# Kernel optimization log

Hardware: AMD Instinct MI355X
Metric: run time of the kernel (lower is better)

Reference implementation:

```python
import jax, jax.numpy as jnp
import numpy as np

B, C, H, W = 64, 256, 32, 32
HID = C // 16          # SE hidden = channels // ratio
EMB = 16               # channel/snr embed dim
COND = 2 * EMB         # cond vector dim = 32
RHID = 64              # rate controller hidden
SNR_DB = 10.0
CH_IDX = 2             # 'Combined_channel'
POWER = 2.0
BASE_CR, MIN_CR, MAX_CR, ALPHA = 0.5, 0.3, 1.0, 0.7


def setup_inputs() -> dict:
    key = jax.random.key(0)
    ks = jax.random.split(key, 16)
    g = lambda k, sh: (jax.random.normal(k, sh, dtype=jnp.float32) * 0.05)
    return {
        "x": jax.random.normal(ks[0], (B, C, H, W), dtype=jnp.float32),
        "channel_embed": g(ks[1], (3, EMB)),
        "snr_w1": g(ks[2], (EMB, 1)), "snr_b1": jnp.zeros((EMB,), jnp.float32),
        "snr_w2": g(ks[3], (EMB, EMB)), "snr_b2": jnp.zeros((EMB,), jnp.float32),
        "base_w1": g(ks[4], (HID, C)),
        "base_w2": g(ks[5], (C, HID)),
        "sem_proj": g(ks[6], (HID, C)),
        "cond_proj": g(ks[7], (HID, COND)),
        "out_proj": g(ks[8], (C, HID)),
        "r_w1": g(ks[9], (RHID, C + COND)), "r_b1": jnp.zeros((RHID,), jnp.float32),
        "r_w2": g(ks[10], (RHID, RHID)), "r_b2": jnp.zeros((RHID,), jnp.float32),
        "r_w3": g(ks[11], (1, RHID)), "r_b3": jnp.zeros((1,), jnp.float32),
    }


def _topk_mask(weights, k):
    # weights [B,C], k [B] int; keep top-k per row (vectorized rank trick).
    order = jnp.argsort(-weights, axis=1)
    ranks = jnp.argsort(order, axis=1)
    return (ranks < k[:, None]).astype(weights.dtype)


def reference(x, channel_embed, snr_w1, snr_b1, snr_w2, snr_b2,
              base_w1, base_w2, sem_proj, cond_proj, out_proj,
              r_w1, r_b1, r_w2, r_b2, r_w3, r_b3):
    b, c, h, w = x.shape
    sem = x.mean(axis=(2, 3))                                   # [B,C] GAP
    # channel condition encoder
    ch_vec = jnp.broadcast_to(channel_embed[CH_IDX], (b, EMB))
    s_in = jnp.full((b, 1), SNR_DB / 28.0, dtype=x.dtype)
    sv = jax.nn.relu(s_in @ snr_w1.T + snr_b1)
    sv = jax.nn.relu(sv @ snr_w2.T + snr_b2)
    cond = jnp.concatenate([ch_vec, sv], axis=1)                # [B,32]
    # base SE weights * channel-conditioned gate
    base = jax.nn.sigmoid(jax.nn.relu(sem @ base_w1.T) @ base_w2.T)
    gate = jax.nn.sigmoid(jax.nn.relu(sem @ sem_proj.T + cond @ cond_proj.T) @ out_proj.T)
    weights = base * gate                                       # [B,C]
    # rate controller -> per-sample cr
    r = jax.nn.relu(jnp.concatenate([sem, cond], axis=1) @ r_w1.T + r_b1)
    r = jax.nn.relu(r @ r_w2.T + r_b2)
    raw = jax.nn.sigmoid(r @ r_w3.T + r_b3)[:, 0]
    dyn = MIN_CR + (MAX_CR - MIN_CR) * raw
    cr = jnp.clip((1.0 - ALPHA) * BASE_CR + ALPHA * dyn, MIN_CR, MAX_CR)
    k = jnp.clip(jnp.round(cr * c).astype(jnp.int32), 1, c)
    mask = _topk_mask(weights, k)
    z = x * (weights * mask)[:, :, None, None]                  # masked latent
    # --- combined channel: flat Rayleigh fading + per-(b,c,h) AWGN ---
    F = c * h * w
    zf = z.reshape(b, F)
    xr, xi = zf[:, 0::2], zf[:, 1::2]                           # [B,F/2]
    nk = jax.random.split(jax.random.key(42), 5)
    hr = jax.random.normal(nk[0], xr.shape, x.dtype)            # torch h_i (real)
    hi = jax.random.normal(nk[1], xr.shape, x.dtype)            # torch h_r (imag)
    std = jnp.sqrt(jnp.asarray(POWER / (10.0 ** (SNR_DB / 10.0)), x.dtype))
    nr = std * jax.random.normal(nk[2], xr.shape, x.dtype)
    ni = std * jax.random.normal(nk[3], xr.shape, x.dtype)
    yr = hr * xr - hi * xi + nr
    yi = hr * xi + hi * xr + ni
    den = hr * hr + hi * hi
    outr = (yr * hr + yi * hi) / den
    outi = (yi * hr - yr * hi) / den
    faded = jnp.stack([outr, outi], axis=-1).reshape(b, c, h, w)
    # per-(b,c,h) random SNR map AWGN
    kk = jax.random.split(nk[4], 2)
    snr_map = jax.random.randint(kk[0], (b, c, h, 1), 0, 29).astype(x.dtype)
    std2 = jnp.sqrt(POWER / (10.0 ** (snr_map / 10.0)))
    return faded + std2 * jax.random.normal(kk[1], (b, c, h, w), x.dtype)
```

## Files before the change

### kernel.cpp

```cpp
#include <hip/hip_runtime.h>

#define NB 64
#define NC 256
#define NF 262144
#define NPAIR 131072
#define NROWS 524288

struct U2 { unsigned a, b; };

__host__ __device__ constexpr unsigned rotl32(unsigned x, int d) {
  return (x << d) | (x >> (32 - d));
}

__host__ __device__ constexpr U2 tf2x32(unsigned k0, unsigned k1,
                                        unsigned x0, unsigned x1) {
  const unsigned ks0 = k0, ks1 = k1, ks2 = k0 ^ k1 ^ 0x1BD11BDAu;
  x0 += ks0; x1 += ks1;
  x0 += x1; x1 = rotl32(x1, 13); x1 ^= x0;
  x0 += x1; x1 = rotl32(x1, 15); x1 ^= x0;
  x0 += x1; x1 = rotl32(x1, 26); x1 ^= x0;
  x0 += x1; x1 = rotl32(x1, 6);  x1 ^= x0;
  x0 += ks1; x1 += ks2 + 1u;
  x0 += x1; x1 = rotl32(x1, 17); x1 ^= x0;
  x0 += x1; x1 = rotl32(x1, 29); x1 ^= x0;
  x0 += x1; x1 = rotl32(x1, 16); x1 ^= x0;
  x0 += x1; x1 = rotl32(x1, 24); x1 ^= x0;
  x0 += ks2; x1 += ks0 + 2u;
  x0 += x1; x1 = rotl32(x1, 13); x1 ^= x0;
  x0 += x1; x1 = rotl32(x1, 15); x1 ^= x0;
  x0 += x1; x1 = rotl32(x1, 26); x1 ^= x0;
  x0 += x1; x1 = rotl32(x1, 6);  x1 ^= x0;
  x0 += ks0; x1 += ks1 + 3u;
  x0 += x1; x1 = rotl32(x1, 17); x1 ^= x0;
  x0 += x1; x1 = rotl32(x1, 29); x1 ^= x0;
  x0 += x1; x1 = rotl32(x1, 16); x1 ^= x0;
  x0 += x1; x1 = rotl32(x1, 24); x1 ^= x0;
  x0 += ks1; x1 += ks2 + 4u;
  x0 += x1; x1 = rotl32(x1, 13); x1 ^= x0;
  x0 += x1; x1 = rotl32(x1, 15); x1 ^= x0;
  x0 += x1; x1 = rotl32(x1, 26); x1 ^= x0;
  x0 += x1; x1 = rotl32(x1, 6);  x1 ^= x0;
  x0 += ks2; x1 += ks0 + 5u;
  return U2{x0, x1};
}

constexpr U2 NK0 = tf2x32(0u, 42u, 0u, 0u);
constexpr U2 NK1 = tf2x32(0u, 42u, 0u, 1u);
constexpr U2 NK2 = tf2x32(0u, 42u, 0u, 2u);
constexpr U2 NK3 = tf2x32(0u, 42u, 0u, 3u);
constexpr U2 NK4 = tf2x32(0u, 42u, 0u, 4u);
constexpr U2 KK0 = tf2x32(NK4.a, NK4.b, 0u, 0u);
constexpr U2 KK1 = tf2x32(NK4.a, NK4.b, 0u, 1u);

__device__ __forceinline__ unsigned rb32(unsigned k0, unsigned k1, unsigned m) {
  const unsigned ks2 = k0 ^ k1 ^ 0x1BD11BDAu;
  unsigned x0 = k0, x1 = m + k1;
#define QR(r) x0 += x1; x1 = __builtin_rotateleft32(x1, r); x1 ^= x0;
  QR(13) QR(15) QR(26) QR(6)
  x0 += k1;  x1 += ks2 + 1u;
  QR(17) QR(29) QR(16) QR(24)
  x0 += ks2; x1 += k0 + 2u;
  QR(13) QR(15) QR(26) QR(6)
  x0 += k0;  x1 += k1 + 3u;
  QR(17) QR(29) QR(16) QR(24)
  x0 += k1;  x1 += ks2 + 4u;
  QR(13) QR(15) QR(26) QR(6)
  x0 += ks2; x1 += k0 + 5u;
#undef QR
  return x0 ^ x1;
}

__device__ __forceinline__ float normal_fast(unsigned bits) {
  const float lo = __uint_as_float(0xBF7FFFFFu);
  float u = __uint_as_float((bits >> 9) | 0x3F800000u) - 1.0f;
  float v = fmaf(u, 2.0f, lo);
  float t = fmaf(-v, v, 1.0f);
  float w = __builtin_amdgcn_logf(t) * -0.69314718f;
  float p;
  if (w < 5.0f) {
    float z = w - 2.5f;
    p = 2.81022636e-08f;
    p = fmaf(p, z, 3.43273939e-07f);
    p = fmaf(p, z, -3.5233877e-06f);
    p = fmaf(p, z, -4.39150654e-06f);
    p = fmaf(p, z, 0.00021858087f);
    p = fmaf(p, z, -0.00125372503f);
    p = fmaf(p, z, -0.00417768164f);
    p = fmaf(p, z, 0.246640727f);
    p = fmaf(p, z, 1.50140941f);
  } else {
    float z = __builtin_amdgcn_sqrtf(w) - 3.0f;
    p = -0.000200214257f;
    p = fmaf(p, z, 0.000100950558f);
    p = fmaf(p, z, 0.00134934322f);
    p = fmaf(p, z, -0.00367342844f);
    p = fmaf(p, z, 0.00573950773f);
    p = fmaf(p, z, -0.0076224613f);
    p = fmaf(p, z, 0.00943887047f);
    p = fmaf(p, z, 1.00167406f);
    p = fmaf(p, z, 2.83297682f);
  }
  return 1.41421356f * (p * v);
}

__global__ __launch_bounds__(256) void snr_kernel(float* __restrict__ std2) {
  const unsigned j = blockIdx.x * 256u + threadIdx.x;
  unsigned hb = rb32(KK0.a, KK0.b, j);
  unsigned lb = rb32(KK0.a, KK0.b, NROWS + j);
  unsigned snr = ((hb % 29u) * 16u + (lb % 29u)) % 29u;
  std2[j] = __builtin_amdgcn_sqrtf(
      2.0f * __builtin_amdgcn_exp2f((float)snr * -0.33219281f));
}

__global__ __launch_bounds__(256) void sem_kernel(const float* __restrict__ x,
                                                  float* __restrict__ sem) {
  int row = (blockIdx.x * 256 + threadIdx.x) >> 6;
  int lane = threadIdx.x & 63;
  const float* rp = x + (size_t)row * 1024;
  float acc = 0.0f;
#pragma unroll
  for (int i = 0; i < 4; ++i) {
    float4 v = *(const float4*)(rp + i * 256 + lane * 4);
    acc += v.x + v.y + v.z + v.w;
  }
#pragma unroll
  for (int off = 32; off > 0; off >>= 1) acc += __shfl_down(acc, off, 64);
  if (lane == 0) sem[row] = acc * (1.0f / 1024.0f);
}

__global__ __launch_bounds__(256) void head_kernel(
    const float* __restrict__ sem_g, const float* __restrict__ channel_embed,
    const float* __restrict__ snr_w1, const float* __restrict__ snr_b1,
    const float* __restrict__ snr_w2, const float* __restrict__ snr_b2,
    const float* __restrict__ base_w1, const float* __restrict__ base_w2,
    const float* __restrict__ sem_proj, const float* __restrict__ cond_proj,
    const float* __restrict__ out_proj, const float* __restrict__ r_w1,
    const float* __restrict__ r_b1, const float* __restrict__ r_w2,
    const float* __restrict__ r_b2, const float* __restrict__ r_w3,
    const float* __restrict__ r_b3, float* __restrict__ s_out) {
  __shared__ float sem_s[256];
  __shared__ float sv1_s[16];
  __shared__ float cond_s[32];
  __shared__ float hid_s[16], g1_s[16];
  __shared__ float r1_s[64], r2_s[64];
  __shared__ float w_s[256];
  __shared__ int k_s;
  const int b = blockIdx.x, t = threadIdx.x;

  sem_s[t] = sem_g[b * 256 + t];
  if (t < 16) {
    const float s_in = (float)(10.0 / 28.0);
    sv1_s[t] = fmaxf(0.0f, s_in * snr_w1[t] + snr_b1[t]);
  }
  __syncthreads();
  if (t < 16) {
    float a = snr_b2[t];
    for (int f = 0; f < 16; ++f) a += sv1_s[f] * snr_w2[t * 16 + f];
    cond_s[16 + t] = fmaxf(0.0f, a);
    cond_s[t] = channel_embed[2 * 16 + t];
  }
  __syncthreads();
  if (t < 16) {
    float a1 = 0.0f, a2 = 0.0f;
    for (int c = 0; c < 256; ++c) {
      float sc = sem_s[c];
      a1 += sc * base_w1[t * 256 + c];
      a2 += sc * sem_proj[t * 256 + c];
    }
    for (int j = 0; j < 32; ++j) a2 += cond_s[j] * cond_proj[t * 32 + j];
    hid_s[t] = fmaxf(0.0f, a1);
    g1_s[t] = fmaxf(0.0f, a2);
  } else if (t < 80) {
    int i = t - 16;
    float a = r_b1[i];
    for (int c = 0; c < 256; ++c) a += sem_s[c] * r_w1[i * 288 + c];
    for (int j = 0; j < 32; ++j) a += cond_s[j] * r_w1[i * 288 + 256 + j];
    r1_s[i] = fmaxf(0.0f, a);
  }
  __syncthreads();
  if (t < 64) {
    float a = r_b2[t];
    for (int j = 0; j < 64; ++j) a += r1_s[j] * r_w2[t * 64 + j];
    r2_s[t] = fmaxf(0.0f, a);
  }
  {
    float a1 = 0.0f, a2 = 0.0f;
    for (int i = 0; i < 16; ++i) {
      a1 += hid_s[i] * base_w2[t * 16 + i];
      a2 += g1_s[i] * out_proj[t * 16 + i];
    }
    float base = 1.0f / (1.0f + expf(-a1));
    float gate = 1.0f / (1.0f + expf(-a2));
    w_s[t] = base * gate;
  }
  __syncthreads();
  if (t == 0) {
    float a = r_b3[0];
    for (int j = 0; j < 64; ++j) a += r2_s[j] * r_w3[j];
    float raw = 1.0f / (1.0f + expf(-a));
    float dyn = 0.3f + 0.7f * raw;
    float cr = 0.15f + 0.7f * dyn;
    cr = fminf(fmaxf(cr, 0.3f), 1.0f);
    int k = (int)rintf(cr * 256.0f);
    k_s = min(max(k, 1), 256);
  }
  __syncthreads();
  {
    float wc = w_s[t];
    int cnt = 0;
    for (int j = 0; j < 256; ++j) {
      float wj = w_s[j];
      cnt += (wj > wc) || (wj == wc && j < t);
    }
    s_out[b * 256 + t] = (cnt < k_s) ? wc : 0.0f;
  }
}

__global__ __launch_bounds__(256) void sim_kernel(const float* __restrict__ x,
                                                  const float* __restrict__ s,
                                                  const float* __restrict__ std2v,
                                                  float* __restrict__ out) {
  const unsigned tid = blockIdx.x * 256u + threadIdx.x;
  const unsigned q0 = tid * 8u;

  const float4 xa = *(const float4*)(x + q0);
  const float4 xb = *(const float4*)(x + q0 + 4);
  const float sc = s[q0 >> 10];
  const float std2 = std2v[q0 >> 5];

  const unsigned m0 = tid * 4u;
  float hr[4], hi[4], nr[4], ni[4], n2[8];
  const float STD = 0.44721359f;
#pragma unroll
  for (int i = 0; i < 4; ++i) hr[i] = normal_fast(rb32(NK0.a, NK0.b, m0 + i));
#pragma unroll
  for (int i = 0; i < 4; ++i) hi[i] = normal_fast(rb32(NK1.a, NK1.b, m0 + i));
#pragma unroll
  for (int i = 0; i < 4; ++i)
    nr[i] = STD * normal_fast(rb32(NK2.a, NK2.b, m0 + i));
#pragma unroll
  for (int i = 0; i < 4; ++i)
    ni[i] = STD * normal_fast(rb32(NK3.a, NK3.b, m0 + i));
#pragma unroll
  for (int i = 0; i < 8; ++i) n2[i] = normal_fast(rb32(KK1.a, KK1.b, q0 + i));

  float xs[8] = {xa.x * sc, xa.y * sc, xa.z * sc, xa.w * sc,
                 xb.x * sc, xb.y * sc, xb.z * sc, xb.w * sc};
  float o[8];
#pragma unroll
  for (int i = 0; i < 4; ++i) {
    const float den = fmaf(hr[i], hr[i], hi[i] * hi[i]);
    const float rc = __builtin_amdgcn_rcpf(den);
    o[2 * i] = fmaf(fmaf(hr[i], nr[i], hi[i] * ni[i]), rc, xs[2 * i]);
    o[2 * i + 1] = fmaf(fmaf(hr[i], ni[i], -(hi[i] * nr[i])), rc, xs[2 * i + 1]);
  }
  float4 oa, ob;
  oa.x = fmaf(std2, n2[0], o[0]);
  oa.y = fmaf(std2, n2[1], o[1]);
  oa.z = fmaf(std2, n2[2], o[2]);
  oa.w = fmaf(std2, n2[3], o[3]);
  ob.x = fmaf(std2, n2[4], o[4]);
  ob.y = fmaf(std2, n2[5], o[5]);
  ob.z = fmaf(std2, n2[6], o[6]);
  ob.w = fmaf(std2, n2[7], o[7]);
  *(float4*)(out + q0) = oa;
  *(float4*)(out + q0 + 4) = ob;
}

extern "C" void kernel_launch(void* const* d_in, const int* in_sizes, int n_in,
                              void* d_out, int out_size, void* d_ws,
                              size_t ws_size, hipStream_t stream) {
  const float* x = (const float*)d_in[0];
  const float* channel_embed = (const float*)d_in[1];
  const float* snr_w1 = (const float*)d_in[2];
  const float* snr_b1 = (const float*)d_in[3];
  const float* snr_w2 = (const float*)d_in[4];
  const float* snr_b2 = (const float*)d_in[5];
  const float* base_w1 = (const float*)d_in[6];
  const float* base_w2 = (const float*)d_in[7];
  const float* sem_proj = (const float*)d_in[8];
  const float* cond_proj = (const float*)d_in[9];
  const float* out_proj = (const float*)d_in[10];
  const float* r_w1 = (const float*)d_in[11];
  const float* r_b1 = (const float*)d_in[12];
  const float* r_w2 = (const float*)d_in[13];
  const float* r_b2 = (const float*)d_in[14];
  const float* r_w3 = (const float*)d_in[15];
  const float* r_b3 = (const float*)d_in[16];

  float* std2 = (float*)d_ws;
  float* sem = std2 + NROWS;
  float* s = sem + NB * NC;

  sem_kernel<<<NB * NC / 4, 256, 0, stream>>>(x, sem);
  snr_kernel<<<NROWS / 256, 256, 0, stream>>>(std2);
  head_kernel<<<NB, 256, 0, stream>>>(sem, channel_embed, snr_w1, snr_b1,
                                      snr_w2, snr_b2, base_w1, base_w2,
                                      sem_proj, cond_proj, out_proj, r_w1,
                                      r_b1, r_w2, r_b2, r_w3, r_b3, s);
  sim_kernel<<<NB * NF / 8 / 256, 256, 0, stream>>>(x, s, std2, (float*)d_out);
}
```

Before: 134.3 us.

## Fuse sem and snr prep kernels, parallelize head GEMVs per wave, fold normal scaling

Merges the GAP reduction and SNR-map generation into one prep launch, removing one kernel launch and its tail. The head kernel now computes its 96 dot products with one 64-lane wave each and a shuffle reduction, instead of serial per-thread loops over 256 inputs. The normal sampler folds the sqrt(2) and noise std scale into the polynomial coefficients and tests the branch on the log value directly, saving a few ALU ops per sample in the main simulation kernel.

```diff
diff --git a/kernel.cpp b/kernel.cpp
--- a/kernel.cpp
+++ b/kernel.cpp
@@ -3,7 +3,6 @@
 #define NB 64
 #define NC 256
 #define NF 262144
-#define NPAIR 131072
 #define NROWS 524288
 
 struct U2 { unsigned a, b; };
@@ -70,62 +69,66 @@
   return x0 ^ x1;
 }
 
+template <int S>
 __device__ __forceinline__ float normal_fast(unsigned bits) {
+  constexpr float K = (S == 0) ? 1.41421356f : 1.41421356f * 0.44721359f;
   const float lo = __uint_as_float(0xBF7FFFFFu);
   float u = __uint_as_float((bits >> 9) | 0x3F800000u) - 1.0f;
   float v = fmaf(u, 2.0f, lo);
   float t = fmaf(-v, v, 1.0f);
-  float w = __builtin_amdgcn_logf(t) * -0.69314718f;
+  float L = __builtin_amdgcn_logf(t);
   float p;
-  if (w < 5.0f) {
-    float z = w - 2.5f;
-    p = 2.81022636e-08f;
-    p = fmaf(p, z, 3.43273939e-07f);
-    p = fmaf(p, z, -3.5233877e-06f);
-    p = fmaf(p, z, -4.39150654e-06f);
-    p = fmaf(p, z, 0.00021858087f);
-    p = fmaf(p, z, -0.00125372503f);
-    p = fmaf(p, z, -0.00417768164f);
-    p = fmaf(p, z, 0.246640727f);
-    p = fmaf(p, z, 1.50140941f);
+  if (L > -7.2134752f) {
+    float z = fmaf(L, -0.69314718f, -2.5f);
+    p = K * 2.81022636e-08f;
+    p = fmaf(p, z, K * 3.43273939e-07f);
+    p = fmaf(p, z, K * -3.5233877e-06f);
+    p = fmaf(p, z, K * -4.39150654e-06f);
+    p = fmaf(p, z, K * 0.00021858087f);
+    p = fmaf(p, z, K * -0.00125372503f);
+    p = fmaf(p, z, K * -0.00417768164f);
+    p = fmaf(p, z, K * 0.246640727f);
+    p = fmaf(p, z, K * 1.50140941f);
   } else {
+    float w = L * -0.69314718f;
     float z = __builtin_amdgcn_sqrtf(w) - 3.0f;
-    p = -0.000200214257f;
-    p = fmaf(p, z, 0.000100950558f);
-    p = fmaf(p, z, 0.00134934322f);
-    p = fmaf(p, z, -0.00367342844f);
-    p = fmaf(p, z, 0.00573950773f);
-    p = fmaf(p, z, -0.0076224613f);
-    p = fmaf(p, z, 0.00943887047f);
-    p = fmaf(p, z, 1.00167406f);
-    p = fmaf(p, z, 2.83297682f);
-  }
-  return 1.41421356f * (p * v);
-}
-
-__global__ __launch_bounds__(256) void snr_kernel(float* __restrict__ std2) {
-  const unsigned j = blockIdx.x * 256u + threadIdx.x;
-  unsigned hb = rb32(KK0.a, KK0.b, j);
-  unsigned lb = rb32(KK0.a, KK0.b, NROWS + j);
-  unsigned snr = ((hb % 29u) * 16u + (lb % 29u)) % 29u;
-  std2[j] = __builtin_amdgcn_sqrtf(
-      2.0f * __builtin_amdgcn_exp2f((float)snr * -0.33219281f));
-}
-
-__global__ __launch_bounds__(256) void sem_kernel(const float* __restrict__ x,
-                                                  float* __restrict__ sem) {
-  int row = (blockIdx.x * 256 + threadIdx.x) >> 6;
-  int lane = threadIdx.x & 63;
-  const float* rp = x + (size_t)row * 1024;
-  float acc = 0.0f;
-#pragma unroll
-  for (int i = 0; i < 4; ++i) {
-    float4 v = *(const float4*)(rp + i * 256 + lane * 4);
-    acc += v.x + v.y + v.z + v.w;
-  }
-#pragma unroll
-  for (int off = 32; off > 0; off >>= 1) acc += __shfl_down(acc, off, 64);
-  if (lane == 0) sem[row] = acc * (1.0f / 1024.0f);
+    p = K * -0.000200214257f;
+    p = fmaf(p, z, K * 0.000100950558f);
+    p = fmaf(p, z, K * 0.00134934322f);
+    p = fmaf(p, z, K * -0.00367342844f);
+    p = fmaf(p, z, K * 0.00573950773f);
+    p = fmaf(p, z, K * -0.0076224613f);
+    p = fmaf(p, z, K * 0.00943887047f);
+    p = fmaf(p, z, K * 1.00167406f);
+    p = fmaf(p, z, K * 2.83297682f);
+  }
+  return p * v;
+}
+
+__global__ __launch_bounds__(256) void prep_kernel(const float* __restrict__ x,
+                                                   float* __restrict__ sem,
+                                                   float* __restrict__ std2) {
+  if (blockIdx.x < 4096) {
+    int row = (blockIdx.x * 256 + threadIdx.x) >> 6;
+    int lane = threadIdx.x & 63;
+    const float* rp = x + (size_t)row * 1024;
+    float acc = 0.0f;
+#pragma unroll
+    for (int i = 0; i < 4; ++i) {
+      float4 v = *(const float4*)(rp + i * 256 + lane * 4);
+      acc += v.x + v.y + v.z + v.w;
+    }
+#pragma unroll
+    for (int off = 32; off > 0; off >>= 1) acc += __shfl_down(acc, off, 64);
+    if (lane == 0) sem[row] = acc * (1.0f / 1024.0f);
+  } else {
+    const unsigned j = (blockIdx.x - 4096u) * 256u + threadIdx.x;
+    unsigned hb = rb32(KK0.a, KK0.b, j);
+    unsigned lb = rb32(KK0.a, KK0.b, NROWS + j);
+    unsigned snr = ((hb % 29u) * 16u + (lb % 29u)) % 29u;
+    std2[j] = __builtin_amdgcn_sqrtf(
+        2.0f * __builtin_amdgcn_exp2f((float)snr * -0.33219281f));
+  }
 }
 
 __global__ __launch_bounds__(256) void head_kernel(
@@ -138,16 +141,16 @@
     const float* __restrict__ r_b1, const float* __restrict__ r_w2,
     const float* __restrict__ r_b2, const float* __restrict__ r_w3,
     const float* __restrict__ r_b3, float* __restrict__ s_out) {
-  __shared__ float sem_s[256];
+  __shared__ float conc_s[288];
   __shared__ float sv1_s[16];
-  __shared__ float cond_s[32];
   __shared__ float hid_s[16], g1_s[16];
   __shared__ float r1_s[64], r2_s[64];
   __shared__ float w_s[256];
   __shared__ int k_s;
   const int b = blockIdx.x, t = threadIdx.x;
-
-  sem_s[t] = sem_g[b * 256 + t];
+  const int wv = t >> 6, ln = t & 63;
+
+  conc_s[t] = sem_g[b * 256 + t];
   if (t < 16) {
     const float s_in = (float)(10.0 / 28.0);
     sv1_s[t] = fmaxf(0.0f, s_in * snr_w1[t] + snr_b1[t]);
@@ -156,28 +159,40 @@
   if (t < 16) {
     float a = snr_b2[t];
     for (int f = 0; f < 16; ++f) a += sv1_s[f] * snr_w2[t * 16 + f];
-    cond_s[16 + t] = fmaxf(0.0f, a);
-    cond_s[t] = channel_embed[2 * 16 + t];
-  }
-  __syncthreads();
-  if (t < 16) {
-    float a1 = 0.0f, a2 = 0.0f;
-    for (int c = 0; c < 256; ++c) {
-      float sc = sem_s[c];
-      a1 += sc * base_w1[t * 256 + c];
-      a2 += sc * sem_proj[t * 256 + c];
-    }
-    for (int j = 0; j < 32; ++j) a2 += cond_s[j] * cond_proj[t * 32 + j];
-    hid_s[t] = fmaxf(0.0f, a1);
-    g1_s[t] = fmaxf(0.0f, a2);
-  } else if (t < 80) {
-    int i = t - 16;
-    float a = r_b1[i];
-    for (int c = 0; c < 256; ++c) a += sem_s[c] * r_w1[i * 288 + c];
-    for (int j = 0; j < 32; ++j) a += cond_s[j] * r_w1[i * 288 + 256 + j];
-    r1_s[i] = fmaxf(0.0f, a);
-  }
-  __syncthreads();
+    conc_s[272 + t] = fmaxf(0.0f, a);
+    conc_s[256 + t] = channel_embed[32 + t];
+  }
+  __syncthreads();
+
+  for (int j = wv; j < 96; j += 4) {
+    float acc = 0.0f;
+    if (j < 16) {
+#pragma unroll
+      for (int k = 0; k < 4; ++k)
+        acc += base_w1[j * 256 + ln + k * 64] * conc_s[ln + k * 64];
+    } else if (j < 32) {
+      int r = j - 16;
+#pragma unroll
+      for (int k = 0; k < 4; ++k)
+        acc += sem_proj[r * 256 + ln + k * 64] * conc_s[ln + k * 64];
+      if (ln < 32) acc += cond_proj[r * 32 + ln] * conc_s[256 + ln];
+    } else {
+      int r = j - 32;
+#pragma unroll
+      for (int k = 0; k < 4; ++k)
+        acc += r_w1[r * 288 + ln + k * 64] * conc_s[ln + k * 64];
+      if (ln < 32) acc += r_w1[r * 288 + 256 + ln] * conc_s[256 + ln];
+    }
+#pragma unroll
+    for (int off = 32; off > 0; off >>= 1) acc += __shfl_xor(acc, off, 64);
+    if (ln == 0) {
+      if (j < 16) hid_s[j] = fmaxf(0.0f, acc);
+      else if (j < 32) g1_s[j - 16] = fmaxf(0.0f, acc);
+      else r1_s[j - 32] = fmaxf(0.0f, acc + r_b1[j - 32]);
+    }
+  }
+  __syncthreads();
+
   if (t < 64) {
     float a = r_b2[t];
     for (int j = 0; j < 64; ++j) a += r1_s[j] * r_w2[t * 64 + j];
@@ -185,6 +200,7 @@
   }
   {
     float a1 = 0.0f, a2 = 0.0f;
+#pragma unroll
     for (int i = 0; i < 16; ++i) {
       a1 += hid_s[i] * base_w2[t * 16 + i];
       a2 += g1_s[i] * out_proj[t * 16 + i];
@@ -230,19 +246,21 @@
 
   const unsigned m0 = tid * 4u;
   float hr[4], hi[4], nr[4], ni[4], n2[8];
-  const float STD = 0.44721359f;
-#pragma unroll
-  for (int i = 0; i < 4; ++i) hr[i] = normal_fast(rb32(NK0.a, NK0.b, m0 + i));
-#pragma unroll
-  for (int i = 0; i < 4; ++i) hi[i] = normal_fast(rb32(NK1.a, NK1.b, m0 + i));
 #pragma unroll
   for (int i = 0; i < 4; ++i)
-    nr[i] = STD * normal_fast(rb32(NK2.a, NK2.b, m0 + i));
+    hr[i] = normal_fast<0>(rb32(NK0.a, NK0.b, m0 + i));
 #pragma unroll
   for (int i = 0; i < 4; ++i)
-    ni[i] = STD * normal_fast(rb32(NK3.a, NK3.b, m0 + i));
-#pragma unroll
-  for (int i = 0; i < 8; ++i) n2[i] = normal_fast(rb32(KK1.a, KK1.b, q0 + i));
+    hi[i] = normal_fast<0>(rb32(NK1.a, NK1.b, m0 + i));
+#pragma unroll
+  for (int i = 0; i < 4; ++i)
+    nr[i] = normal_fast<1>(rb32(NK2.a, NK2.b, m0 + i));
+#pragma unroll
+  for (int i = 0; i < 4; ++i)
+    ni[i] = normal_fast<1>(rb32(NK3.a, NK3.b, m0 + i));
+#pragma unroll
+  for (int i = 0; i < 8; ++i)
+    n2[i] = normal_fast<0>(rb32(KK1.a, KK1.b, q0 + i));
 
   float xs[8] = {xa.x * sc, xa.y * sc, xa.z * sc, xa.w * sc,
                  xb.x * sc, xb.y * sc, xb.z * sc, xb.w * sc};
@@ -252,7 +270,8 @@
     const float den = fmaf(hr[i], hr[i], hi[i] * hi[i]);
     const float rc = __builtin_amdgcn_rcpf(den);
     o[2 * i] = fmaf(fmaf(hr[i], nr[i], hi[i] * ni[i]), rc, xs[2 * i]);
-    o[2 * i + 1] = fmaf(fmaf(hr[i], ni[i], -(hi[i] * nr[i])), rc, xs[2 * i + 1]);
+    o[2 * i + 1] =
+        fmaf(fmaf(hr[i], ni[i], -(hi[i] * nr[i])), rc, xs[2 * i + 1]);
   }
   float4 oa, ob;
   oa.x = fmaf(std2, n2[0], o[0]);
@@ -292,8 +311,7 @@
   float* sem = std2 + NROWS;
   float* s = sem + NB * NC;
 
-  sem_kernel<<<NB * NC / 4, 256, 0, stream>>>(x, sem);
-  snr_kernel<<<NROWS / 256, 256, 0, stream>>>(std2);
+  prep_kernel<<<4096 + NROWS / 256, 256, 0, stream>>>(x, sem, std2);
   head_kernel<<<NB, 256, 0, stream>>>(sem, channel_embed, snr_w1, snr_b1,
                                       snr_w2, snr_b2, base_w1, base_w2,
                                       sem_proj, cond_proj, out_proj, r_w1,
```

Result: slower. 140.6 us (+4.7%).
